# Performance work log

Hardware: AMD Instinct MI355X
Metric: run time of the kernel (lower is better)

The kernel has to match this reference:

```python
import jax, jax.numpy as jnp
import numpy as np

N = 12288      # 12 * nside^2, nside=32
NBR = 20       # HEALpix graph neighbors
E = N * (NBR + 1)
B = 4
CIN = 8
COUT = 8
EPS = 1e-5


def _spmm(vals, row, col, x):
    """y = L @ x per batch/channel. x: [B, V, C]; L sparse COO (row, col, vals)."""
    b, v, c = x.shape
    x2 = x.transpose(1, 0, 2).reshape(v, b * c)          # [V, B*C]
    y = jax.ops.segment_sum(x2[col] * vals[:, None], row, num_segments=v)
    return y.reshape(v, b, c).transpose(1, 0, 2)          # [B, V, C]


def _cheb(vals, row, col, x, w, bias):
    """Chebyshev spectral graph conv: sum_k T_k(L) x W_k + b. w: [K, Fin, Fout]."""
    K = w.shape[0]
    xs = [x]
    if K > 1:
        xs.append(_spmm(vals, row, col, x))
    for _ in range(2, K):
        xs.append(2.0 * _spmm(vals, row, col, xs[-1]) - xs[-2])
    xk = jnp.stack(xs)                                    # [K, B, V, Fin]
    return jnp.einsum('kbvi,kio->bvo', xk, w) + bias


def _bn(x, g, b):
    # BatchNorm1d in training mode: stats over (batch, vertex) per channel
    m = x.mean(axis=(0, 1))
    v = x.var(axis=(0, 1))
    return (x - m) * jax.lax.rsqrt(v + EPS) * g + b


def setup_inputs() -> dict:
    key = jax.random.key(0)
    ks = jax.random.split(key, 12)
    x = jax.random.normal(ks[0], (B, N, CIN), jnp.float32)
    row = jnp.repeat(jnp.arange(N, dtype=jnp.int32), NBR + 1)
    nbr = jax.random.randint(ks[1], (N, NBR), 0, N, dtype=jnp.int32)
    col = jnp.concatenate([jnp.arange(N, dtype=jnp.int32)[:, None], nbr], axis=1).reshape(-1)
    edge_val = jax.random.normal(ks[2], (E,), jnp.float32) * 0.1

    def w(k, shape):
        return jax.random.normal(k, shape, jnp.float32) * 0.05

    return dict(
        x=x, edge_row=row, edge_col=col, edge_val=edge_val,
        conv1_w=w(ks[3], (3, CIN, 64)), conv1_b=jnp.zeros((64,), jnp.float32),
        bn1_g=jnp.ones((64,), jnp.float32), bn1_b=jnp.zeros((64,), jnp.float32),
        conv2_w=w(ks[4], (3, 64, 256)), conv2_b=jnp.zeros((256,), jnp.float32),
        bn2_g=jnp.ones((256,), jnp.float32), bn2_b=jnp.zeros((256,), jnp.float32),
        # 3 identical-shape bottlenecks stacked on leading axis
        bt_c1w=w(ks[5], (3, 1, 256, 64)), bt_c1b=jnp.zeros((3, 64), jnp.float32),
        bt_c2w=w(ks[6], (3, 3, 64, 64)), bt_c2b=jnp.zeros((3, 64), jnp.float32),
        bt_c3w=w(ks[7], (3, 1, 64, 256)), bt_c3b=jnp.zeros((3, 256), jnp.float32),
        bt_bn1g=jnp.ones((3, 64), jnp.float32), bt_bn1b=jnp.zeros((3, 64), jnp.float32),
        bt_bn2g=jnp.ones((3, 64), jnp.float32), bt_bn2b=jnp.zeros((3, 64), jnp.float32),
        bt_bn3g=jnp.ones((3, 256), jnp.float32), bt_bn3b=jnp.zeros((3, 256), jnp.float32),
        conv3_w=w(ks[8], (3, 256, COUT)), conv3_b=jnp.zeros((COUT,), jnp.float32),
    )


def reference(x, edge_row, edge_col, edge_val,
              conv1_w, conv1_b, bn1_g, bn1_b,
              conv2_w, conv2_b, bn2_g, bn2_b,
              bt_c1w, bt_c1b, bt_c2w, bt_c2b, bt_c3w, bt_c3b,
              bt_bn1g, bt_bn1b, bt_bn2g, bt_bn2b, bt_bn3g, bt_bn3b,
              conv3_w, conv3_b):
    L = (edge_val, edge_row, edge_col)

    def conv_block(h, w_, b_, g, bb):
        h = _cheb(*L, h, w_, b_)
        return jax.nn.relu(_bn(h, g, bb))

    def bottleneck(h, i):
        y = _cheb(*L, h, bt_c1w[i], bt_c1b[i])
        y = jax.nn.relu(_bn(y, bt_bn1g[i], bt_bn1b[i]))
        y = _cheb(*L, y, bt_c2w[i], bt_c2b[i])
        y = jax.nn.relu(_bn(y, bt_bn2g[i], bt_bn2b[i]))
        y = _cheb(*L, y, bt_c3w[i], bt_c3b[i])
        return _bn(y, bt_bn3g[i], bt_bn3b[i])

    h = conv_block(x, conv1_w, conv1_b, bn1_g, bn1_b)
    h = conv_block(h, conv2_w, conv2_b, bn2_g, bn2_b)
    for i in range(3):  # fixed, structurally distinct bottleneck blocks
        h = h + bottleneck(h, i)
    return _cheb(*L, h, conv3_w, conv3_b)  # [B, N, COUT]
```

## Files before the change

kernel.cpp:

```cpp
#include <hip/hip_runtime.h>

static constexpr int NBRS = 21;
static constexpr int Nv   = 12288;
static constexpr int BV   = 4 * Nv;
static constexpr float BN_EPS = 1e-5f;

typedef __bf16 bf16x4 __attribute__((ext_vector_type(4)));
typedef __bf16 bf16x8 __attribute__((ext_vector_type(8)));
typedef float  f32x4  __attribute__((ext_vector_type(4)));

template<int MODE>
__global__ void spmm8_kernel(float* __restrict__ y, const float* __restrict__ x,
                             const float* __restrict__ x0, const float* __restrict__ x1,
                             const float* __restrict__ val, const int* __restrict__ col)
{
    int idx = blockIdx.x * 256 + threadIdx.x;
    int c = idx % 8;
    int v = (idx / 8) % Nv;
    int b = idx / (8 * Nv);
    int e0 = v * NBRS;
    float acc = 0.f;
    #pragma unroll
    for (int j = 0; j < NBRS; ++j) {
        int u = col[e0 + j];
        acc = fmaf(val[e0 + j], x[((size_t)b * Nv + u) * 8 + c], acc);
    }
    if (MODE == 0)      y[idx] = acc;
    else if (MODE == 1) y[idx] = 2.f * acc - x0[idx];
    else if (MODE == 2) y[idx] = fmaf(2.f, acc, x0[idx]);
    else                y[idx] = acc + x0[idx] - x1[idx];
}

template<bool CHEB2, bool BNG, bool BNX0>
__global__ __launch_bounds__(256)
void spmm64_kernel(__bf16* __restrict__ y, const __bf16* __restrict__ x,
                   const __bf16* __restrict__ x0,
                   const float* __restrict__ val, const int* __restrict__ col,
                   const float* __restrict__ bn_a, const float* __restrict__ bn_b)
{
    int idx = blockIdx.x * 256 + threadIdx.x;
    int q = idx % 16;
    int v = (idx / 16) % Nv;
    int b = idx / (16 * Nv);
    int e0 = v * NBRS;
    const bf16x4* x4 = (const bf16x4*)x;
    float4 a4, b4;
    if (BNG || (CHEB2 && BNX0)) {
        a4 = ((const float4*)bn_a)[q];
        b4 = ((const float4*)bn_b)[q];
    }
    float4 acc = {0.f, 0.f, 0.f, 0.f};
    #pragma unroll
    for (int j = 0; j < NBRS; ++j) {
        int u = col[e0 + j];
        float a = val[e0 + j];
        bf16x4 hv = x4[(size_t)(b * Nv + u) * 16 + q];
        float x0v = (float)hv[0], x1v = (float)hv[1], x2v = (float)hv[2], x3v = (float)hv[3];
        if (BNG) {
            x0v = fmaxf(fmaf(x0v, a4.x, b4.x), 0.f);
            x1v = fmaxf(fmaf(x1v, a4.y, b4.y), 0.f);
            x2v = fmaxf(fmaf(x2v, a4.z, b4.z), 0.f);
            x3v = fmaxf(fmaf(x3v, a4.w, b4.w), 0.f);
        }
        acc.x = fmaf(a, x0v, acc.x);
        acc.y = fmaf(a, x1v, acc.y);
        acc.z = fmaf(a, x2v, acc.z);
        acc.w = fmaf(a, x3v, acc.w);
    }
    if (CHEB2) {
        bf16x4 pv4 = ((const bf16x4*)x0)[idx];
        float p0 = (float)pv4[0], p1 = (float)pv4[1], p2 = (float)pv4[2], p3 = (float)pv4[3];
        if (BNX0) {
            p0 = fmaxf(fmaf(p0, a4.x, b4.x), 0.f);
            p1 = fmaxf(fmaf(p1, a4.y, b4.y), 0.f);
            p2 = fmaxf(fmaf(p2, a4.z, b4.z), 0.f);
            p3 = fmaxf(fmaf(p3, a4.w, b4.w), 0.f);
        }
        acc.x = 2.f * acc.x - p0;
        acc.y = 2.f * acc.y - p1;
        acc.z = 2.f * acc.z - p2;
        acc.w = 2.f * acc.w - p3;
    }
    bf16x4 o;
    o[0] = (__bf16)acc.x; o[1] = (__bf16)acc.y; o[2] = (__bf16)acc.z; o[3] = (__bf16)acc.w;
    ((bf16x4*)y)[idx] = o;
}

__global__ void pack_conv3_kernel(const float* __restrict__ w, const float* __restrict__ bias,
                                  float* __restrict__ wpack, float* __restrict__ bpack)
{
    int t = blockIdx.x * 256 + threadIdx.x;
    if (t < 256 * 32) {
        int ki = t / 32, c = t % 32;
        int j = c / 8, o = c % 8;
        wpack[t] = (j < 3) ? w[(size_t)j * 2048 + ki * 8 + o] : 0.f;
    }
    if (t < 32) bpack[t] = (t < 8) ? bias[t] : 0.f;
}

__global__ __launch_bounds__(256)
void pack_all_kernel(const float* __restrict__ w1, const float* __restrict__ w2,
                     const float* __restrict__ c1, const float* __restrict__ c2,
                     const float* __restrict__ c3, const float* __restrict__ wpk,
                     __bf16* __restrict__ wb)
{
    int t = blockIdx.x * 256 + threadIdx.x;
    if (t >= 194560) return;
    const float* src; int KSRC, FOUT, local;
    if (t < 2048)        { src = w1;  KSRC = 24;  FOUT = 64;  local = t; }
    else if (t < 51200)  { src = w2;  KSRC = 192; FOUT = 256; local = t - 2048; }
    else if (t < 100352) { int i = (t - 51200) / 16384;  src = c1 + (size_t)i * 16384;
                           KSRC = 256; FOUT = 64;  local = (t - 51200) % 16384; }
    else if (t < 137216) { int i = (t - 100352) / 12288; src = c2 + (size_t)i * 12288;
                           KSRC = 192; FOUT = 64;  local = (t - 100352) % 12288; }
    else if (t < 186368) { int i = (t - 137216) / 16384; src = c3 + (size_t)i * 16384;
                           KSRC = 64;  FOUT = 256; local = (t - 137216) % 16384; }
    else                 { src = wpk; KSRC = 256; FOUT = 32;  local = t - 186368; }
    const int j    = local & 7;
    const int lane = (local >> 3) & 63;
    const int rest = local >> 9;
    const int NT = FOUT >> 4;
    const int nt = rest % NT;
    const int ks = rest / NT;
    const int k = ks * 32 + (lane >> 4) * 8 + j;
    const int o = nt * 16 + (lane & 15);
    wb[t] = (k < KSRC) ? (__bf16)src[(size_t)k * FOUT + o] : (__bf16)0.f;
}

template<int FOUT, int KFIN, int KPAD, int FIN, int NSRC,
         bool STATS, bool BN0, bool HAS_BIAS, bool PACKOUT, bool INBF, bool OUTBF,
         bool RESID = false>
__global__ __launch_bounds__(256)
void gemm_mfma_kernel(const void* __restrict__ x0, const void* __restrict__ x1,
                      const void* __restrict__ x2,
                      const __bf16* __restrict__ wp, const float* __restrict__ bias,
                      const float* __restrict__ bn_a, const float* __restrict__ bn_b,
                      void* __restrict__ out, float2* __restrict__ partial)
{
    constexpr int NT    = FOUT / 16;
    constexpr int NSTEP = KPAD / 32;
    constexpr bool COLS = (NT % 4 == 0);
    constexpr int NT2   = COLS ? NT / 4 : NT;
    constexpr int LDKB  = KPAD + 8;
    constexpr int LDC   = FOUT + 4;
    constexpr size_t XS_B  = (size_t)64 * LDKB * 2;
    constexpr size_t RPK_B = COLS ? (size_t)16 * LDC * 4 : 0;
    constexpr size_t SMEM  = XS_B > RPK_B ? XS_B : RPK_B;
    __shared__ __align__(16) char smem[SMEM];
    __bf16* xs = (__bf16*)smem;

    const int tid = threadIdx.x;
    const int m0 = blockIdx.x * 64;

    constexpr int NF4 = 64 * (KPAD / 4);
    for (int f = tid; f < NF4; f += 256) {
        const int r  = f / (KPAD / 4);
        const int ki = (f % (KPAD / 4)) * 4;
        bf16x4 h;
        if (KFIN == KPAD || ki < KFIN) {
            int i; int kk;
            if constexpr (NSRC == 1) { i = ki; kk = 0; }
            else { kk = ki / FIN; i = ki % FIN; }
            if constexpr (RESID) {
                const __bf16* srcy = (const __bf16*)x0;
                const __bf16* srct = (const __bf16*)x1;
                bf16x4 hy = *(const bf16x4*)(srcy + (size_t)(m0 + r) * FIN + i);
                bf16x4 ht = *(const bf16x4*)(srct + (size_t)(m0 + r) * FIN + i);
                const float4 a4 = *(const float4*)(bn_a + i);
                const float4 b4 = *(const float4*)(bn_b + i);
                h[0] = (__bf16)(fmaf((float)hy[0], a4.x, b4.x) + (float)ht[0]);
                h[1] = (__bf16)(fmaf((float)hy[1], a4.y, b4.y) + (float)ht[1]);
                h[2] = (__bf16)(fmaf((float)hy[2], a4.z, b4.z) + (float)ht[2]);
                h[3] = (__bf16)(fmaf((float)hy[3], a4.w, b4.w) + (float)ht[3]);
            } else if constexpr (INBF) {
                const __bf16* src = (kk == 0) ? (const __bf16*)x0
                                  : (kk == 1 ? (const __bf16*)x1 : (const __bf16*)x2);
                bf16x4 hv = *(const bf16x4*)(src + (size_t)(m0 + r) * FIN + i);
                if (BN0 && (NSRC == 1 || kk == 0)) {
                    const float4 a4 = *(const float4*)(bn_a + i);
                    const float4 b4 = *(const float4*)(bn_b + i);
                    h[0] = (__bf16)fmaxf(fmaf((float)hv[0], a4.x, b4.x), 0.f);
                    h[1] = (__bf16)fmaxf(fmaf((float)hv[1], a4.y, b4.y), 0.f);
                    h[2] = (__bf16)fmaxf(fmaf((float)hv[2], a4.z, b4.z), 0.f);
                    h[3] = (__bf16)fmaxf(fmaf((float)hv[3], a4.w, b4.w), 0.f);
                } else {
                    h = hv;
                }
            } else {
                const float* src = (kk == 0) ? (const float*)x0
                                 : (kk == 1 ? (const float*)x1 : (const float*)x2);
                float4 v = *(const float4*)(src + (size_t)(m0 + r) * FIN + i);
                if (BN0 && (NSRC == 1 || kk == 0)) {
                    const float4 a4 = *(const float4*)(bn_a + i);
                    const float4 b4 = *(const float4*)(bn_b + i);
                    v.x = fmaxf(fmaf(v.x, a4.x, b4.x), 0.f);
                    v.y = fmaxf(fmaf(v.y, a4.y, b4.y), 0.f);
                    v.z = fmaxf(fmaf(v.z, a4.z, b4.z), 0.f);
                    v.w = fmaxf(fmaf(v.w, a4.w, b4.w), 0.f);
                }
                h[0] = (__bf16)v.x; h[1] = (__bf16)v.y; h[2] = (__bf16)v.z; h[3] = (__bf16)v.w;
            }
        } else {
            h[0] = (__bf16)0.f; h[1] = (__bf16)0.f; h[2] = (__bf16)0.f; h[3] = (__bf16)0.f;
        }
        *(bf16x4*)(xs + (size_t)r * LDKB + ki) = h;
    }
    __syncthreads();

    const int lane = tid & 63;
    const int wv   = tid >> 6;
    const int lo   = lane & 15;
    const int hi   = lane >> 4;

    if constexpr (COLS) {
        f32x4 acc[4][NT2];
        #pragma unroll
        for (int mr = 0; mr < 4; ++mr)
            #pragma unroll
            for (int n = 0; n < NT2; ++n) acc[mr][n] = (f32x4){0.f, 0.f, 0.f, 0.f};

        #pragma unroll
        for (int ks = 0; ks < NSTEP; ++ks) {
            bf16x8 bfr[NT2];
            #pragma unroll
            for (int n = 0; n < NT2; ++n)
                bfr[n] = *(const bf16x8*)(wp + ((size_t)(ks * NT + wv * NT2 + n) * 64 + lane) * 8);
            bf16x8 afr[4];
            #pragma unroll
            for (int mr = 0; mr < 4; ++mr)
                afr[mr] = *(const bf16x8*)(xs + (size_t)(mr * 16 + lo) * LDKB + ks * 32 + hi * 8);
            #pragma unroll
            for (int n = 0; n < NT2; ++n)
                #pragma unroll
                for (int mr = 0; mr < 4; ++mr)
                    acc[mr][n] = __builtin_amdgcn_mfma_f32_16x16x32_bf16(afr[mr], bfr[n], acc[mr][n], 0, 0, 0);
        }

        #pragma unroll
        for (int n = 0; n < NT2; ++n) {
            const int o = wv * (FOUT / 4) + n * 16 + lo;
            const float bo = HAS_BIAS ? bias[o] : 0.f;
            #pragma unroll
            for (int mr = 0; mr < 4; ++mr)
                #pragma unroll
                for (int j = 0; j < 4; ++j) acc[mr][n][j] += bo;
        }

        if constexpr (STATS) {
            #pragma unroll
            for (int n = 0; n < NT2; ++n) {
                float s = 0.f, q = 0.f;
                #pragma unroll
                for (int mr = 0; mr < 4; ++mr)
                    #pragma unroll
                    for (int j = 0; j < 4; ++j) {
                        const float v = acc[mr][n][j];
                        s += v; q = fmaf(v, v, q);
                    }
                s += __shfl_xor(s, 16); q += __shfl_xor(q, 16);
                s += __shfl_xor(s, 32); q += __shfl_xor(q, 32);
                if (lane < 16) {
                    const int o = wv * (FOUT / 4) + n * 16 + lo;
                    partial[(size_t)o * gridDim.x + blockIdx.x] = make_float2(s, q);
                }
            }
        }

        float* cs = (float*)smem;
        #pragma unroll
        for (int mr = 0; mr < 4; ++mr) {
            __syncthreads();
            #pragma unroll
            for (int n = 0; n < NT2; ++n) {
                const int o = wv * (FOUT / 4) + n * 16 + lo;
                #pragma unroll
                for (int j = 0; j < 4; ++j)
                    cs[(size_t)(hi * 4 + j) * LDC + o] = acc[mr][n][j];
            }
            __syncthreads();
            for (int t = tid; t < 16 * (FOUT / 4); t += 256) {
                const int rr = t / (FOUT / 4);
                const int c4 = (t % (FOUT / 4)) * 4;
                const float4 v = *(const float4*)(cs + (size_t)rr * LDC + c4);
                if constexpr (OUTBF) {
                    bf16x4 hv;
                    hv[0] = (__bf16)v.x; hv[1] = (__bf16)v.y;
                    hv[2] = (__bf16)v.z; hv[3] = (__bf16)v.w;
                    *(bf16x4*)((__bf16*)out + (size_t)(m0 + mr * 16 + rr) * FOUT + c4) = hv;
                } else {
                    *(float4*)((float*)out + (size_t)(m0 + mr * 16 + rr) * FOUT + c4) = v;
                }
            }
        }
    } else {
        f32x4 acc[NT];
        #pragma unroll
        for (int nt = 0; nt < NT; ++nt) acc[nt] = (f32x4){0.f, 0.f, 0.f, 0.f};
        const int arow = wv * 16 + lo;
        #pragma unroll
        for (int ks = 0; ks < NSTEP; ++ks) {
            const bf16x8 a = *(const bf16x8*)(xs + (size_t)arow * LDKB + ks * 32 + hi * 8);
            #pragma unroll
            for (int nt = 0; nt < NT; ++nt) {
                const bf16x8 b = *(const bf16x8*)(wp + ((size_t)(ks * NT + nt) * 64 + lane) * 8);
                acc[nt] = __builtin_amdgcn_mfma_f32_16x16x32_bf16(a, b, acc[nt], 0, 0, 0);
            }
        }
        #pragma unroll
        for (int nt = 0; nt < NT; ++nt) {
            const int o = nt * 16 + lo;
            const float bo = HAS_BIAS ? bias[o] : 0.f;
            #pragma unroll
            for (int j = 0; j < 4; ++j) {
                const float v = acc[nt][j] + bo;
                const int m = m0 + wv * 16 + hi * 4 + j;
                if constexpr (PACKOUT) {
                    const int zj = o >> 3;
                    if (zj < 3) ((float*)out)[((size_t)zj * BV + m) * 8 + (o & 7)] = v;
                } else {
                    ((float*)out)[(size_t)m * FOUT + o] = v;
                }
            }
        }
    }
}

__global__ __launch_bounds__(256)
void bn_finalize_kernel(const float2* __restrict__ partial,
                        const float* __restrict__ g, const float* __restrict__ b,
                        float* __restrict__ a_out, float* __restrict__ b_out,
                        float invN, int nblk)
{
    __shared__ float2 red[4];
    const int c = blockIdx.x;
    const float2* p = partial + (size_t)c * nblk;
    float s = 0.f, ss = 0.f;
    for (int k = threadIdx.x; k < nblk; k += 256) {
        const float2 v = p[k];
        s += v.x; ss += v.y;
    }
    #pragma unroll
    for (int off = 32; off > 0; off >>= 1) {
        s  += __shfl_down(s, off);
        ss += __shfl_down(ss, off);
    }
    if ((threadIdx.x & 63) == 0) red[threadIdx.x >> 6] = make_float2(s, ss);
    __syncthreads();
    if (threadIdx.x == 0) {
        float ts = 0.f, tq = 0.f;
        #pragma unroll
        for (int i = 0; i < 4; ++i) { ts += red[i].x; tq += red[i].y; }
        const float m = ts * invN;
        const float var = tq * invN - m * m;
        const float a = g[c] * rsqrtf(var + BN_EPS);
        a_out[c] = a;
        b_out[c] = b[c] - m * a;
    }
}

template<int C, bool BASEBN>
__global__ __launch_bounds__(256)
void bn_apply_kernel(__bf16* __restrict__ out, const __bf16* __restrict__ x,
                     const __bf16* __restrict__ base,
                     const float* __restrict__ bn_a, const float* __restrict__ bn_b,
                     const float* __restrict__ bn_a2, const float* __restrict__ bn_b2)
{
    int i = blockIdx.x * 256 + threadIdx.x;
    bf16x4 hv = ((const bf16x4*)x)[i];
    int c0 = (i * 4) % C;
    float4 a4 = *reinterpret_cast<const float4*>(bn_a + c0);
    float4 b4 = *reinterpret_cast<const float4*>(bn_b + c0);
    float r0 = fmaf((float)hv[0], a4.x, b4.x);
    float r1 = fmaf((float)hv[1], a4.y, b4.y);
    float r2 = fmaf((float)hv[2], a4.z, b4.z);
    float r3 = fmaf((float)hv[3], a4.w, b4.w);
    bf16x4 bb = ((const bf16x4*)base)[i];
    float v0 = (float)bb[0], v1 = (float)bb[1], v2 = (float)bb[2], v3 = (float)bb[3];
    if (BASEBN) {
        float4 p4 = *reinterpret_cast<const float4*>(bn_a2 + c0);
        float4 q4 = *reinterpret_cast<const float4*>(bn_b2 + c0);
        v0 = fmaxf(fmaf(v0, p4.x, q4.x), 0.f);
        v1 = fmaxf(fmaf(v1, p4.y, q4.y), 0.f);
        v2 = fmaxf(fmaf(v2, p4.z, q4.z), 0.f);
        v3 = fmaxf(fmaf(v3, p4.w, q4.w), 0.f);
    }
    bf16x4 o;
    o[0] = (__bf16)(r0 + v0);
    o[1] = (__bf16)(r1 + v1);
    o[2] = (__bf16)(r2 + v2);
    o[3] = (__bf16)(r3 + v3);
    ((bf16x4*)out)[i] = o;
}

extern "C" void kernel_launch(void* const* d_in, const int* in_sizes, int n_in,
                              void* d_out, int out_size, void* d_ws, size_t ws_size,
                              hipStream_t stream)
{
    const float* x       = (const float*)d_in[0];
    const int*   col     = (const int*)  d_in[2];
    const float* eval_   = (const float*)d_in[3];
    const float* conv1_w = (const float*)d_in[4];
    const float* conv1_b = (const float*)d_in[5];
    const float* bn1_g   = (const float*)d_in[6];
    const float* bn1_b   = (const float*)d_in[7];
    const float* conv2_w = (const float*)d_in[8];
    const float* conv2_b = (const float*)d_in[9];
    const float* bn2_g   = (const float*)d_in[10];
    const float* bn2_b   = (const float*)d_in[11];
    const float* bt_c1w  = (const float*)d_in[12];
    const float* bt_c1b  = (const float*)d_in[13];
    const float* bt_c2w  = (const float*)d_in[14];
    const float* bt_c2b  = (const float*)d_in[15];
    const float* bt_c3w  = (const float*)d_in[16];
    const float* bt_c3b  = (const float*)d_in[17];
    const float* btbn1g  = (const float*)d_in[18];
    const float* btbn1b  = (const float*)d_in[19];
    const float* btbn2g  = (const float*)d_in[20];
    const float* btbn2b  = (const float*)d_in[21];
    const float* btbn3g  = (const float*)d_in[22];
    const float* btbn3b  = (const float*)d_in[23];
    const float* conv3_w = (const float*)d_in[24];
    const float* conv3_b = (const float*)d_in[25];
    float* out = (float*)d_out;

    __bf16* h2b  = (__bf16*)d_ws;
    __bf16* y3b  = h2b + (size_t)BV * 256;
    __bf16* t64a = y3b + (size_t)BV * 256;
    __bf16* t64b = t64a + (size_t)BV * 64;
    __bf16* t64c = t64b + (size_t)BV * 64;
    __bf16* t64d = t64c + (size_t)BV * 64;
    float*  scr  = (float*)(t64d + (size_t)BV * 64);
    float*  aarr = scr + (size_t)BV * 32;
    float*  barr = aarr + 11 * 256;
    float*  wpack = barr + 11 * 256;
    float*  bpack = wpack + 256 * 32;
    __bf16* wb   = (__bf16*)(bpack + 32);
    __bf16* wp1  = wb;
    __bf16* wp2  = wp1 + 2048;
    __bf16* wpc1 = wp2 + 49152;
    __bf16* wpc2 = wpc1 + 49152;
    __bf16* wpc3 = wpc2 + 36864;
    __bf16* wp3  = wpc3 + 49152;
    float2* part = (float2*)(wp3 + 8192);

    float* t8a = scr;
    float* t8b = scr + (size_t)BV * 8;

    const float invN = 1.f / (float)BV;
    const int NGB  = BV / 64;
    const int NSP64 = BV * 16 / 256;

    pack_conv3_kernel<<<32, 256, 0, stream>>>(conv3_w, conv3_b, wpack, bpack);
    pack_all_kernel<<<760, 256, 0, stream>>>(conv1_w, conv2_w, bt_c1w, bt_c2w, bt_c3w, wpack, wb);

    spmm8_kernel<0><<<BV * 8 / 256, 256, 0, stream>>>(t8a, x, nullptr, nullptr, eval_, col);
    spmm8_kernel<1><<<BV * 8 / 256, 256, 0, stream>>>(t8b, t8a, x, nullptr, eval_, col);
    gemm_mfma_kernel<64, 24, 32, 8, 3, true, false, true, false, false, true>
        <<<NGB, 256, 0, stream>>>(x, t8a, t8b, wp1, conv1_b, nullptr, nullptr, t64c, part);
    bn_finalize_kernel<<<64, 256, 0, stream>>>(part, bn1_g, bn1_b, aarr, barr, invN, NGB);

    spmm64_kernel<false, true, false><<<NSP64, 256, 0, stream>>>(t64a, t64c, nullptr, eval_, col, aarr, barr);
    spmm64_kernel<true, false, true ><<<NSP64, 256, 0, stream>>>(t64b, t64a, t64c, eval_, col, aarr, barr);
    gemm_mfma_kernel<256, 192, 192, 64, 3, true, true, true, false, true, true>
        <<<NGB, 256, 0, stream>>>(t64c, t64a, t64b, wp2, conv2_b, aarr, barr, h2b, part);
    bn_finalize_kernel<<<256, 256, 0, stream>>>(part, bn2_g, bn2_b, aarr + 256, barr + 256, invN, NGB);

    for (int i = 0; i < 3; ++i) {
        float* aA = aarr + (2 + i * 3) * 256; float* bA = barr + (2 + i * 3) * 256;
        float* aB = aarr + (3 + i * 3) * 256; float* bB = barr + (3 + i * 3) * 256;
        float* aC = aarr + (4 + i * 3) * 256; float* bC = barr + (4 + i * 3) * 256;

        if (i == 0)
            gemm_mfma_kernel<64, 256, 256, 256, 1, true, true, true, false, true, true>
                <<<NGB, 256, 0, stream>>>(h2b, nullptr, nullptr, wpc1,
                                          bt_c1b, aarr + 256, barr + 256, t64c, part);
        else
            gemm_mfma_kernel<64, 256, 256, 256, 1, true, false, true, false, true, true>
                <<<NGB, 256, 0, stream>>>(h2b, nullptr, nullptr, wpc1 + (size_t)i * 16384,
                                          bt_c1b + i * 64, nullptr, nullptr, t64c, part);
        bn_finalize_kernel<<<64, 256, 0, stream>>>(part, btbn1g + i * 64, btbn1b + i * 64, aA, bA, invN, NGB);

        spmm64_kernel<false, true, false><<<NSP64, 256, 0, stream>>>(t64a, t64c, nullptr, eval_, col, aA, bA);
        spmm64_kernel<true, false, true ><<<NSP64, 256, 0, stream>>>(t64b, t64a, t64c, eval_, col, aA, bA);
        gemm_mfma_kernel<64, 192, 192, 64, 3, true, true, true, false, true, true>
            <<<NGB, 256, 0, stream>>>(t64c, t64a, t64b, wpc2 + (size_t)i * 12288,
                                      bt_c2b + i * 64, aA, bA, t64d, part);
        bn_finalize_kernel<<<64, 256, 0, stream>>>(part, btbn2g + i * 64, btbn2b + i * 64, aB, bB, invN, NGB);

        gemm_mfma_kernel<256, 64, 64, 64, 1, true, true, true, false, true, true>
            <<<NGB, 256, 0, stream>>>(t64d, nullptr, nullptr, wpc3 + (size_t)i * 16384,
                                      bt_c3b + i * 256, aB, bB, y3b, part);
        bn_finalize_kernel<<<256, 256, 0, stream>>>(part, btbn3g + i * 256, btbn3b + i * 256, aC, bC, invN, NGB);

        if (i == 0)
            bn_apply_kernel<256, true><<<BV / 4, 256, 0, stream>>>(
                h2b, y3b, h2b, aC, bC, aarr + 256, barr + 256);
        else if (i == 1)
            bn_apply_kernel<256, false><<<BV / 4, 256, 0, stream>>>(
                h2b, y3b, h2b, aC, bC, nullptr, nullptr);
    }

    float* z0 = scr;
    float* z1 = z0 + (size_t)BV * 8;
    float* z2 = z1 + (size_t)BV * 8;
    float* ee = z2 + (size_t)BV * 8;
    float* aC2 = aarr + 10 * 256;
    float* bC2 = barr + 10 * 256;

    gemm_mfma_kernel<32, 256, 256, 256, 1, false, true, true, true, true, false, true>
        <<<NGB, 256, 0, stream>>>(y3b, h2b, nullptr, wp3, bpack, aC2, bC2, z0, nullptr);

    spmm8_kernel<2><<<BV * 8 / 256, 256, 0, stream>>>(ee, z2, z1, nullptr, eval_, col);
    spmm8_kernel<3><<<BV * 8 / 256, 256, 0, stream>>>(out, ee, z0, z2, eval_, col);

    (void)in_sizes; (void)n_in; (void)out_size; (void)ws_size;
}
```

Before: 341.4 us.

## Widen SpMM gathers to 16-byte vectors and fuse conv3 weight packing

The 8-channel SpMM now has each thread handle four channels with float4 gathers, and the 64-channel SpMM has each thread handle eight bf16 values with 16-byte loads. This cuts the thread count and the per-thread index and value loads, so each gathered row costs fewer memory transactions. The separate conv3 packing kernel is folded into pack_all_kernel, which drops one launch and one intermediate buffer. The trade-off is higher register use per thread and fewer threads to hide gather latency.

```diff
diff --git a/kernel.cpp b/kernel.cpp
--- a/kernel.cpp
+++ b/kernel.cpp
@@ -10,25 +10,44 @@
 typedef float  f32x4  __attribute__((ext_vector_type(4)));
 
 template<int MODE>
-__global__ void spmm8_kernel(float* __restrict__ y, const float* __restrict__ x,
-                             const float* __restrict__ x0, const float* __restrict__ x1,
-                             const float* __restrict__ val, const int* __restrict__ col)
+__global__ __launch_bounds__(256)
+void spmm8_kernel(float* __restrict__ y, const float* __restrict__ x,
+                  const float* __restrict__ x0, const float* __restrict__ x1,
+                  const float* __restrict__ val, const int* __restrict__ col)
 {
     int idx = blockIdx.x * 256 + threadIdx.x;
-    int c = idx % 8;
-    int v = (idx / 8) % Nv;
-    int b = idx / (8 * Nv);
+    int c4 = idx & 1;
+    int row = idx >> 1;
+    int v = row % Nv;
+    int b = row / Nv;
     int e0 = v * NBRS;
-    float acc = 0.f;
+    const float4* x4 = (const float4*)x;
+    float4 acc = {0.f, 0.f, 0.f, 0.f};
     #pragma unroll
     for (int j = 0; j < NBRS; ++j) {
         int u = col[e0 + j];
-        acc = fmaf(val[e0 + j], x[((size_t)b * Nv + u) * 8 + c], acc);
-    }
-    if (MODE == 0)      y[idx] = acc;
-    else if (MODE == 1) y[idx] = 2.f * acc - x0[idx];
-    else if (MODE == 2) y[idx] = fmaf(2.f, acc, x0[idx]);
-    else                y[idx] = acc + x0[idx] - x1[idx];
+        float a = val[e0 + j];
+        float4 xv = x4[(size_t)(b * Nv + u) * 2 + c4];
+        acc.x = fmaf(a, xv.x, acc.x);
+        acc.y = fmaf(a, xv.y, acc.y);
+        acc.z = fmaf(a, xv.z, acc.z);
+        acc.w = fmaf(a, xv.w, acc.w);
+    }
+    if (MODE == 1) {
+        float4 p = ((const float4*)x0)[idx];
+        acc.x = 2.f * acc.x - p.x; acc.y = 2.f * acc.y - p.y;
+        acc.z = 2.f * acc.z - p.z; acc.w = 2.f * acc.w - p.w;
+    } else if (MODE == 2) {
+        float4 p = ((const float4*)x0)[idx];
+        acc.x = fmaf(2.f, acc.x, p.x); acc.y = fmaf(2.f, acc.y, p.y);
+        acc.z = fmaf(2.f, acc.z, p.z); acc.w = fmaf(2.f, acc.w, p.w);
+    } else if (MODE == 3) {
+        float4 p = ((const float4*)x0)[idx];
+        float4 q = ((const float4*)x1)[idx];
+        acc.x += p.x - q.x; acc.y += p.y - q.y;
+        acc.z += p.z - q.z; acc.w += p.w - q.w;
+    }
+    ((float4*)y)[idx] = acc;
 }
 
 template<bool CHEB2, bool BNG, bool BNX0>
@@ -39,74 +58,78 @@
                    const float* __restrict__ bn_a, const float* __restrict__ bn_b)
 {
     int idx = blockIdx.x * 256 + threadIdx.x;
-    int q = idx % 16;
-    int v = (idx / 16) % Nv;
-    int b = idx / (16 * Nv);
+    int q = idx % 8;
+    int v = (idx / 8) % Nv;
+    int b = idx / (8 * Nv);
     int e0 = v * NBRS;
-    const bf16x4* x4 = (const bf16x4*)x;
-    float4 a4, b4;
+    const bf16x8* x8 = (const bf16x8*)x;
+    float4 aL, aH, bL, bH;
     if (BNG || (CHEB2 && BNX0)) {
-        a4 = ((const float4*)bn_a)[q];
-        b4 = ((const float4*)bn_b)[q];
-    }
-    float4 acc = {0.f, 0.f, 0.f, 0.f};
+        aL = ((const float4*)bn_a)[q * 2];     aH = ((const float4*)bn_a)[q * 2 + 1];
+        bL = ((const float4*)bn_b)[q * 2];     bH = ((const float4*)bn_b)[q * 2 + 1];
+    }
+    float acc[8];
+    #pragma unroll
+    for (int t = 0; t < 8; ++t) acc[t] = 0.f;
     #pragma unroll
     for (int j = 0; j < NBRS; ++j) {
         int u = col[e0 + j];
         float a = val[e0 + j];
-        bf16x4 hv = x4[(size_t)(b * Nv + u) * 16 + q];
-        float x0v = (float)hv[0], x1v = (float)hv[1], x2v = (float)hv[2], x3v = (float)hv[3];
+        bf16x8 hv = x8[(size_t)(b * Nv + u) * 8 + q];
+        float xv[8];
+        #pragma unroll
+        for (int t = 0; t < 8; ++t) xv[t] = (float)hv[t];
         if (BNG) {
-            x0v = fmaxf(fmaf(x0v, a4.x, b4.x), 0.f);
-            x1v = fmaxf(fmaf(x1v, a4.y, b4.y), 0.f);
-            x2v = fmaxf(fmaf(x2v, a4.z, b4.z), 0.f);
-            x3v = fmaxf(fmaf(x3v, a4.w, b4.w), 0.f);
-        }
-        acc.x = fmaf(a, x0v, acc.x);
-        acc.y = fmaf(a, x1v, acc.y);
-        acc.z = fmaf(a, x2v, acc.z);
-        acc.w = fmaf(a, x3v, acc.w);
+            xv[0] = fmaxf(fmaf(xv[0], aL.x, bL.x), 0.f);
+            xv[1] = fmaxf(fmaf(xv[1], aL.y, bL.y), 0.f);
+            xv[2] = fmaxf(fmaf(xv[2], aL.z, bL.z), 0.f);
+            xv[3] = fmaxf(fmaf(xv[3], aL.w, bL.w), 0.f);
+            xv[4] = fmaxf(fmaf(xv[4], aH.x, bH.x), 0.f);
+            xv[5] = fmaxf(fmaf(xv[5], aH.y, bH.y), 0.f);
+            xv[6] = fmaxf(fmaf(xv[6], aH.z, bH.z), 0.f);
+            xv[7] = fmaxf(fmaf(xv[7], aH.w, bH.w), 0.f);
+        }
+        #pragma unroll
+        for (int t = 0; t < 8; ++t) acc[t] = fmaf(a, xv[t], acc[t]);
     }
     if (CHEB2) {
-        bf16x4 pv4 = ((const bf16x4*)x0)[idx];
-        float p0 = (float)pv4[0], p1 = (float)pv4[1], p2 = (float)pv4[2], p3 = (float)pv4[3];
+        bf16x8 pv = ((const bf16x8*)x0)[idx];
+        float p[8];
+        #pragma unroll
+        for (int t = 0; t < 8; ++t) p[t] = (float)pv[t];
         if (BNX0) {
-            p0 = fmaxf(fmaf(p0, a4.x, b4.x), 0.f);
-            p1 = fmaxf(fmaf(p1, a4.y, b4.y), 0.f);
-            p2 = fmaxf(fmaf(p2, a4.z, b4.z), 0.f);
-            p3 = fmaxf(fmaf(p3, a4.w, b4.w), 0.f);
-        }
-        acc.x = 2.f * acc.x - p0;
-        acc.y = 2.f * acc.y - p1;
-        acc.z = 2.f * acc.z - p2;
-        acc.w = 2.f * acc.w - p3;
-    }
-    bf16x4 o;
-    o[0] = (__bf16)acc.x; o[1] = (__bf16)acc.y; o[2] = (__bf16)acc.z; o[3] = (__bf16)acc.w;
-    ((bf16x4*)y)[idx] = o;
-}
-
-__global__ void pack_conv3_kernel(const float* __restrict__ w, const float* __restrict__ bias,
-                                  float* __restrict__ wpack, float* __restrict__ bpack)
-{
-    int t = blockIdx.x * 256 + threadIdx.x;
-    if (t < 256 * 32) {
-        int ki = t / 32, c = t % 32;
-        int j = c / 8, o = c % 8;
-        wpack[t] = (j < 3) ? w[(size_t)j * 2048 + ki * 8 + o] : 0.f;
-    }
-    if (t < 32) bpack[t] = (t < 8) ? bias[t] : 0.f;
+            p[0] = fmaxf(fmaf(p[0], aL.x, bL.x), 0.f);
+            p[1] = fmaxf(fmaf(p[1], aL.y, bL.y), 0.f);
+            p[2] = fmaxf(fmaf(p[2], aL.z, bL.z), 0.f);
+            p[3] = fmaxf(fmaf(p[3], aL.w, bL.w), 0.f);
+            p[4] = fmaxf(fmaf(p[4], aH.x, bH.x), 0.f);
+            p[5] = fmaxf(fmaf(p[5], aH.y, bH.y), 0.f);
+            p[6] = fmaxf(fmaf(p[6], aH.z, bH.z), 0.f);
+            p[7] = fmaxf(fmaf(p[7], aH.w, bH.w), 0.f);
+        }
+        #pragma unroll
+        for (int t = 0; t < 8; ++t) acc[t] = 2.f * acc[t] - p[t];
+    }
+    bf16x8 o;
+    #pragma unroll
+    for (int t = 0; t < 8; ++t) o[t] = (__bf16)acc[t];
+    ((bf16x8*)y)[idx] = o;
 }
 
 __global__ __launch_bounds__(256)
 void pack_all_kernel(const float* __restrict__ w1, const float* __restrict__ w2,
                      const float* __restrict__ c1, const float* __restrict__ c2,
-                     const float* __restrict__ c3, const float* __restrict__ wpk,
-                     __bf16* __restrict__ wb)
+                     const float* __restrict__ c3, const float* __restrict__ w3,
+                     const float* __restrict__ b3,
+                     __bf16* __restrict__ wb, float* __restrict__ bpack)
 {
     int t = blockIdx.x * 256 + threadIdx.x;
-    if (t >= 194560) return;
-    const float* src; int KSRC, FOUT, local;
+    if (t >= 194560) {
+        int i = t - 194560;
+        if (i < 32) bpack[i] = (i < 8) ? b3[i] : 0.f;
+        return;
+    }
+    const float* src; int KSRC, FOUT, local; bool isW3 = false;
     if (t < 2048)        { src = w1;  KSRC = 24;  FOUT = 64;  local = t; }
     else if (t < 51200)  { src = w2;  KSRC = 192; FOUT = 256; local = t - 2048; }
     else if (t < 100352) { int i = (t - 51200) / 16384;  src = c1 + (size_t)i * 16384;
@@ -115,7 +138,7 @@
                            KSRC = 192; FOUT = 64;  local = (t - 100352) % 12288; }
     else if (t < 186368) { int i = (t - 137216) / 16384; src = c3 + (size_t)i * 16384;
                            KSRC = 64;  FOUT = 256; local = (t - 137216) % 16384; }
-    else                 { src = wpk; KSRC = 256; FOUT = 32;  local = t - 186368; }
+    else                 { src = w3;  KSRC = 256; FOUT = 32;  local = t - 186368; isW3 = true; }
     const int j    = local & 7;
     const int lane = (local >> 3) & 63;
     const int rest = local >> 9;
@@ -124,7 +147,13 @@
     const int ks = rest / NT;
     const int k = ks * 32 + (lane >> 4) * 8 + j;
     const int o = nt * 16 + (lane & 15);
-    wb[t] = (k < KSRC) ? (__bf16)src[(size_t)k * FOUT + o] : (__bf16)0.f;
+    float v;
+    if (isW3) {
+        v = (o < 24) ? src[(size_t)(o >> 3) * 2048 + k * 8 + (o & 7)] : 0.f;
+    } else {
+        v = (k < KSRC) ? src[(size_t)k * FOUT + o] : 0.f;
+    }
+    wb[t] = (__bf16)v;
 }
 
 template<int FOUT, int KFIN, int KPAD, int FIN, int NSRC,
@@ -432,8 +461,7 @@
     float*  scr  = (float*)(t64d + (size_t)BV * 64);
     float*  aarr = scr + (size_t)BV * 32;
     float*  barr = aarr + 11 * 256;
-    float*  wpack = barr + 11 * 256;
-    float*  bpack = wpack + 256 * 32;
+    float*  bpack = barr + 11 * 256;
     __bf16* wb   = (__bf16*)(bpack + 32);
     __bf16* wp1  = wb;
     __bf16* wp2  = wp1 + 2048;
@@ -448,13 +476,14 @@
 
     const float invN = 1.f / (float)BV;
     const int NGB  = BV / 64;
-    const int NSP64 = BV * 16 / 256;
-
-    pack_conv3_kernel<<<32, 256, 0, stream>>>(conv3_w, conv3_b, wpack, bpack);
-    pack_all_kernel<<<760, 256, 0, stream>>>(conv1_w, conv2_w, bt_c1w, bt_c2w, bt_c3w, wpack, wb);
-
-    spmm8_kernel<0><<<BV * 8 / 256, 256, 0, stream>>>(t8a, x, nullptr, nullptr, eval_, col);
-    spmm8_kernel<1><<<BV * 8 / 256, 256, 0, stream>>>(t8b, t8a, x, nullptr, eval_, col);
+    const int NSP64 = BV * 8 / 256;
+    const int NSP8  = BV * 2 / 256;
+
+    pack_all_kernel<<<761, 256, 0, stream>>>(conv1_w, conv2_w, bt_c1w, bt_c2w, bt_c3w,
+                                             conv3_w, conv3_b, wb, bpack);
+
+    spmm8_kernel<0><<<NSP8, 256, 0, stream>>>(t8a, x, nullptr, nullptr, eval_, col);
+    spmm8_kernel<1><<<NSP8, 256, 0, stream>>>(t8b, t8a, x, nullptr, eval_, col);
     gemm_mfma_kernel<64, 24, 32, 8, 3, true, false, true, false, false, true>
         <<<NGB, 256, 0, stream>>>(x, t8a, t8b, wp1, conv1_b, nullptr, nullptr, t64c, part);
     bn_finalize_kernel<<<64, 256, 0, stream>>>(part, bn1_g, bn1_b, aarr, barr, invN, NGB);
@@ -510,8 +539,8 @@
     gemm_mfma_kernel<32, 256, 256, 256, 1, false, true, true, true, true, false, true>
         <<<NGB, 256, 0, stream>>>(y3b, h2b, nullptr, wp3, bpack, aC2, bC2, z0, nullptr);
 
-    spmm8_kernel<2><<<BV * 8 / 256, 256, 0, stream>>>(ee, z2, z1, nullptr, eval_, col);
-    spmm8_kernel<3><<<BV * 8 / 256, 256, 0, stream>>>(out, ee, z0, z2, eval_, col);
+    spmm8_kernel<2><<<NSP8, 256, 0, stream>>>(ee, z2, z1, nullptr, eval_, col);
+    spmm8_kernel<3><<<NSP8, 256, 0, stream>>>(out, ee, z0, z2, eval_, col);
 
     (void)in_sizes; (void)n_in; (void)out_size; (void)ws_size;
 }
```

Result: faster. 334.5 us (-2.0%).
